# Optimization experiments

Hardware: AMD Instinct MI355X
Metric: run time of the kernel (lower is better)

## Reference

```python
import jax, jax.numpy as jnp
import numpy as np
import math

D_MODEL = 1024
N_HEADS = 16
DK = D_MODEL // N_HEADS


def setup_inputs() -> dict:
    key = jax.random.key(0)
    kx, kqkv, kproj = jax.random.split(key, 3)
    B, T = 4, 2048
    x = jax.random.normal(kx, (B, T, D_MODEL), dtype=jnp.float32)
    # torch Linear weight is [out, in]; y = x @ W.T
    W_qkv = jax.random.normal(kqkv, (3 * D_MODEL, D_MODEL), dtype=jnp.float32) * (1.0 / math.sqrt(D_MODEL))
    W_proj = jax.random.normal(kproj, (D_MODEL, D_MODEL), dtype=jnp.float32) * (1.0 / math.sqrt(D_MODEL))
    return {"x": x, "W_qkv": W_qkv, "W_proj": W_proj}


def reference(x, W_qkv, W_proj):
    B, T, D = x.shape
    qkv = jnp.einsum("btd,ed->bte", x, W_qkv)  # [B,T,3D]
    q, k, v = jnp.split(qkv, 3, axis=-1)
    # [B,T,D] -> [B,H,T,dk]
    def heads(t):
        return t.reshape(B, T, N_HEADS, DK).transpose(0, 2, 1, 3)
    q, k, v = heads(q), heads(k), heads(v)
    scale = 1.0 / math.sqrt(DK)
    att = jnp.einsum("bhqd,bhkd->bhqk", q, k) * scale  # [B,H,T,T]
    att = jax.nn.softmax(att, axis=-1)
    out = jnp.einsum("bhqk,bhkd->bhqd", att, v)  # [B,H,T,dk]
    out = out.transpose(0, 2, 1, 3).reshape(B, T, D)
    return jnp.einsum("btd,ed->bte", out, W_proj)
```

## Files before the change

### kernel.cpp

```cpp
#include <hip/hip_runtime.h>
#include <hip/hip_bf16.h>

#define D_MODEL 1024
#define N_HEADS 16
#define DK 64
#define B_SZ 4
#define T_SEQ 2048
#define M_ROWS (B_SZ * T_SEQ)
#define QK_SCALE_LOG2 0.18033688f

#define XN ((size_t)M_ROWS * D_MODEL)
#define WQ ((size_t)3 * D_MODEL * D_MODEL)
#define WP ((size_t)D_MODEL * D_MODEL)

typedef short bf16x8 __attribute__((ext_vector_type(8)));
typedef float f32x4  __attribute__((ext_vector_type(4)));

__device__ inline unsigned short f32_to_bf16(float f) {
    union { float f; unsigned int u; } v; v.f = f;
    unsigned int r = v.u + 0x7fff + ((v.u >> 16) & 1);
    return (unsigned short)(r >> 16);
}
__device__ inline unsigned int pack_bf16x2(float a, float b) {
    __hip_bfloat162 t = __float22bfloat162_rn(make_float2(a, b));
    union { __hip_bfloat162 v; unsigned int u; } c; c.v = t;
    return c.u;
}

__global__ __launch_bounds__(256) void cast_all(
    const float* __restrict__ x, const float* __restrict__ W_qkv,
    const float* __restrict__ W_proj,
    unsigned short* __restrict__ xb, unsigned short* __restrict__ wqb,
    unsigned short* __restrict__ wpb)
{
    const size_t total = (XN + WQ + WP) / 4;
    for (size_t i4 = blockIdx.x * 256 + threadIdx.x; i4 < total;
         i4 += gridDim.x * 256) {
        const size_t i = i4 * 4;
        const float* src; unsigned short* dst; float sc = 1.0f; size_t off;
        if (i < XN) {
            src = x; dst = xb; off = i;
        } else if (i < XN + WQ) {
            off = i - XN; src = W_qkv; dst = wqb;
            if (off < (size_t)D_MODEL * D_MODEL) sc = QK_SCALE_LOG2;
        } else {
            off = i - XN - WQ; src = W_proj; dst = wpb;
        }
        float4 v = *(const float4*)(src + off);
        ushort4 h;
        h.x = f32_to_bf16(v.x * sc); h.y = f32_to_bf16(v.y * sc);
        h.z = f32_to_bf16(v.z * sc); h.w = f32_to_bf16(v.w * sc);
        *(ushort4*)(dst + off) = h;
    }
}

template <typename OutT, bool FUSE_VT>
__global__ __launch_bounds__(256, 4) void gemm_bf16_nt(
    const unsigned short* __restrict__ A, const unsigned short* __restrict__ B,
    OutT* __restrict__ C, unsigned short* __restrict__ vt,
    int M, int N, int K)
{
    __shared__ __align__(16) unsigned short sA[128 * 64];
    __shared__ __align__(16) unsigned short sB[128 * 64];

    const int t    = threadIdx.x;
    const int wave = t >> 6;
    const int lane = t & 63;
    const int l15  = lane & 15;
    const int quad = lane >> 4;
    const int swz  = l15 & 7;

    const int cpx = gridDim.x >> 3;
    const int wg  = (blockIdx.x & 7) * cpx + (blockIdx.x >> 3);
    const int nbm = M >> 7;
    const int n0  = (wg / nbm) * 128;
    const int m0  = (wg % nbm) * 128;

    const unsigned short* gplane = (wave < 2) ? A : B;
    unsigned short* lplane = (wave < 2) ? sA : sB;
    const int row0 = ((wave < 2) ? m0 : n0) + (wave & 1) * 64;
    unsigned short* lbase = lplane + (wave & 1) * 4096;
    const int rsub = lane >> 3;
    const int cg   = (lane & 7) ^ rsub;
    const unsigned short* gbase =
        gplane + (size_t)(row0 + rsub) * K + cg * 8;

    f32x4 acc[4][4];
#pragma unroll
    for (int i = 0; i < 4; ++i)
#pragma unroll
        for (int j = 0; j < 4; ++j) acc[i][j] = (f32x4){0.f, 0.f, 0.f, 0.f};

    const int wr = (wave >> 1) * 64;
    const int wc = (wave & 1) * 64;

    for (int k0 = 0; k0 < K; k0 += 64) {
#pragma unroll
        for (int i = 0; i < 8; ++i) {
            __builtin_amdgcn_global_load_lds(
                (const __attribute__((address_space(1))) unsigned int*)
                    (gbase + k0 + (size_t)(i * 8) * K),
                (__attribute__((address_space(3))) unsigned int*)
                    (lbase + i * 512),
                16, 0, 0);
        }
        __syncthreads();

#pragma unroll
        for (int kk = 0; kk < 2; ++kk) {
            bf16x8 a[4], b[4];
            const int ch = kk * 4 + quad;
            const int co = (ch ^ swz) * 8;
#pragma unroll
            for (int f = 0; f < 4; ++f) {
                a[f] = *(const bf16x8*)&sA[(wr + f * 16 + l15) * 64 + co];
                b[f] = *(const bf16x8*)&sB[(wc + f * 16 + l15) * 64 + co];
            }
#pragma unroll
            for (int mi = 0; mi < 4; ++mi)
#pragma unroll
                for (int ni = 0; ni < 4; ++ni)
                    acc[mi][ni] = __builtin_amdgcn_mfma_f32_16x16x32_bf16(
                        a[mi], b[ni], acc[mi][ni], 0, 0, 0);
        }
        __syncthreads();
    }

    if constexpr (FUSE_VT) {
        if (n0 >= 2 * D_MODEL) {
            const int bb   = m0 >> 11;
            const int tile = (m0 & 2047) >> 7;
            const int hA   = (n0 + wc - 2 * D_MODEL) >> 6;
            unsigned short* vtile =
                vt + ((size_t)((bb * N_HEADS + hA) * (T_SEQ / 128) + tile))
                     * (16 * 64 * 8);
            const int chi = (wr >> 6) * 8;
#pragma unroll
            for (int cc = 0; cc < 2; ++cc) {
                const int c   = chi + cc * 4 + quad;
                const int mi0 = 2 * cc;
#pragma unroll
                for (int ni = 0; ni < 4; ++ni) {
                    const int d = ni * 16 + l15;
                    uint4 p;
                    p.x = pack_bf16x2(acc[mi0][ni][0],     acc[mi0][ni][1]);
                    p.y = pack_bf16x2(acc[mi0][ni][2],     acc[mi0][ni][3]);
                    p.z = pack_bf16x2(acc[mi0 + 1][ni][0], acc[mi0 + 1][ni][1]);
                    p.w = pack_bf16x2(acc[mi0 + 1][ni][2], acc[mi0 + 1][ni][3]);
                    *(uint4*)(vtile + (c * 64 + d) * 8) = p;
                }
            }
            return;
        }
    }

#pragma unroll
    for (int mi = 0; mi < 4; ++mi)
#pragma unroll
        for (int r = 0; r < 4; ++r) {
            OutT* crow =
                C + (size_t)(m0 + wr + mi * 16 + quad * 4 + r) * N + n0 + wc + l15;
#pragma unroll
            for (int ni = 0; ni < 4; ++ni) {
                if constexpr (sizeof(OutT) == 2)
                    crow[ni * 16] = (OutT)f32_to_bf16(acc[mi][ni][r]);
                else
                    crow[ni * 16] = (OutT)acc[mi][ni][r];
            }
        }
}

__global__ __launch_bounds__(256, 4) void attn_mfma(
    const unsigned short* __restrict__ qkvb,
    const unsigned short* __restrict__ vt,
    unsigned short* __restrict__ ob)
{
    __shared__ __align__(16) unsigned short Ksw[2][128 * 64];

    const int t    = threadIdx.x;
    const int wave = t >> 6;
    const int lane = t & 63;
    const int l15  = t & 15;
    const int quad = lane >> 4;
    const int swz  = l15 & 7;

    const int b  = blockIdx.z;
    const int h  = blockIdx.y;
    const int q0 = blockIdx.x * 128;

    bf16x8 qa[2][2];
#pragma unroll
    for (int qs = 0; qs < 2; ++qs) {
        const unsigned short* qrow =
            qkvb + ((size_t)(b * T_SEQ) + q0 + wave * 32 + qs * 16 + l15)
                   * (3 * D_MODEL) + h * DK;
        qa[qs][0] = *(const bf16x8*)(qrow + quad * 8);
        qa[qs][1] = *(const bf16x8*)(qrow + 32 + quad * 8);
    }

    f32x4 O[2][4], Lacc[2];
#pragma unroll
    for (int qs = 0; qs < 2; ++qs) {
        Lacc[qs] = (f32x4){0.f, 0.f, 0.f, 0.f};
#pragma unroll
        for (int nd = 0; nd < 4; ++nd) O[qs][nd] = (f32x4){0.f, 0.f, 0.f, 0.f};
    }

    const short one_bf = (short)0x3F80;
    const bf16x8 ones8 = {one_bf, one_bf, one_bf, one_bf,
                          one_bf, one_bf, one_bf, one_bf};

    const unsigned short* kbase =
        qkvb + (size_t)(b * T_SEQ) * (3 * D_MODEL) + D_MODEL + h * DK;
    const unsigned short* vbase =
        vt + (size_t)(b * N_HEADS + h) * DK * T_SEQ;

    const int krl  = wave * 32 + (lane >> 3);
    const int kcol = ((lane & 7) ^ (lane >> 3)) * 8;

#pragma unroll
    for (int i = 0; i < 4; ++i) {
        const int rk = krl + i * 8;
        __builtin_amdgcn_global_load_lds(
            (const __attribute__((address_space(1))) unsigned int*)
                (kbase + (size_t)rk * (3 * D_MODEL) + kcol),
            (__attribute__((address_space(3))) unsigned int*)
                (&Ksw[0][(wave * 4 + i) * 512]),
            16, 0, 0);
    }

    const int NT = T_SEQ / 128;
    for (int tile = 0; tile < NT; ++tile) {
        __syncthreads();

        if (tile + 1 < NT) {
            const int c0n = (tile + 1) * 128;
            const int nb  = (tile + 1) & 1;
#pragma unroll
            for (int i = 0; i < 4; ++i) {
                const int rk = krl + i * 8;
                __builtin_amdgcn_global_load_lds(
                    (const __attribute__((address_space(1))) unsigned int*)
                        (kbase + (size_t)(c0n + rk) * (3 * D_MODEL) + kcol),
                    (__attribute__((address_space(3))) unsigned int*)
                        (&Ksw[nb][(wave * 4 + i) * 512]),
                    16, 0, 0);
            }
        }

        const int cb = tile & 1;
        const unsigned short* vtile = vbase + (size_t)tile * (16 * 64 * 8);
        const unsigned short* vlane = vtile + quad * 512 + l15 * 8;
#pragma unroll
        for (int half = 0; half < 2; ++half) {
            f32x4 S[2][4];
#pragma unroll
            for (int qs = 0; qs < 2; ++qs)
#pragma unroll
                for (int nf = 0; nf < 4; ++nf) S[qs][nf] = (f32x4){0.f, 0.f, 0.f, 0.f};

            __builtin_amdgcn_s_setprio(1);
#pragma unroll
            for (int ks = 0; ks < 2; ++ks) {
                const int ch = ks * 4 + quad;
#pragma unroll
                for (int nf = 0; nf < 4; ++nf) {
                    const int row = half * 64 + nf * 16 + l15;
                    const bf16x8 kf =
                        *(const bf16x8*)&Ksw[cb][row * 64 + ((ch ^ swz) * 8)];
                    S[0][nf] = __builtin_amdgcn_mfma_f32_16x16x32_bf16(
                        kf, qa[0][ks], S[0][nf], 0, 0, 0);
                    S[1][nf] = __builtin_amdgcn_mfma_f32_16x16x32_bf16(
                        kf, qa[1][ks], S[1][nf], 0, 0, 0);
                }
            }
            __builtin_amdgcn_s_setprio(0);

#pragma unroll
            for (int gl = 0; gl < 2; ++gl) {
                bf16x8 pf[2];
#pragma unroll
                for (int qs = 0; qs < 2; ++qs) {
                    union { uint4 u; bf16x8 v; } cv;
                    const f32x4 s0 = S[qs][2 * gl];
                    const f32x4 s1 = S[qs][2 * gl + 1];
                    cv.u.x = pack_bf16x2(__builtin_amdgcn_exp2f(s0[0]),
                                         __builtin_amdgcn_exp2f(s0[1]));
                    cv.u.y = pack_bf16x2(__builtin_amdgcn_exp2f(s0[2]),
                                         __builtin_amdgcn_exp2f(s0[3]));
                    cv.u.z = pack_bf16x2(__builtin_amdgcn_exp2f(s1[0]),
                                         __builtin_amdgcn_exp2f(s1[1]));
                    cv.u.w = pack_bf16x2(__builtin_amdgcn_exp2f(s1[2]),
                                         __builtin_amdgcn_exp2f(s1[3]));
                    pf[qs] = cv.v;
                }
                const int g = half * 2 + gl;
                const unsigned short* vptr = vlane + (size_t)g * 2048;
                __builtin_amdgcn_s_setprio(1);
#pragma unroll
                for (int nd = 0; nd < 4; ++nd) {
                    const bf16x8 vb = *(const bf16x8*)(vptr + nd * 128);
                    O[0][nd] = __builtin_amdgcn_mfma_f32_16x16x32_bf16(
                        pf[0], vb, O[0][nd], 0, 0, 0);
                    O[1][nd] = __builtin_amdgcn_mfma_f32_16x16x32_bf16(
                        pf[1], vb, O[1][nd], 0, 0, 0);
                }
                Lacc[0] = __builtin_amdgcn_mfma_f32_16x16x32_bf16(
                    pf[0], ones8, Lacc[0], 0, 0, 0);
                Lacc[1] = __builtin_amdgcn_mfma_f32_16x16x32_bf16(
                    pf[1], ones8, Lacc[1], 0, 0, 0);
                __builtin_amdgcn_s_setprio(0);
            }
        }
    }

#pragma unroll
    for (int qs = 0; qs < 2; ++qs)
#pragma unroll
        for (int r = 0; r < 4; ++r) {
            const float invl = 1.0f / Lacc[qs][r];
            const size_t rowbase =
                ((size_t)(b * T_SEQ) + q0 + wave * 32 + qs * 16 + quad * 4 + r)
                * D_MODEL + h * DK + l15;
#pragma unroll
            for (int nd = 0; nd < 4; ++nd)
                ob[rowbase + nd * 16] = f32_to_bf16(O[qs][nd][r] * invl);
        }
}

extern "C" void kernel_launch(void* const* d_in, const int* in_sizes, int n_in,
                              void* d_out, int out_size, void* d_ws, size_t ws_size,
                              hipStream_t stream)
{
    const float* x      = (const float*)d_in[0];
    const float* W_qkv  = (const float*)d_in[1];
    const float* W_proj = (const float*)d_in[2];
    float* out = (float*)d_out;

    unsigned short* xb   = (unsigned short*)d_ws;
    unsigned short* wqb  = xb + XN;
    unsigned short* wpb  = wqb + WQ;
    unsigned short* qkvb = wpb + WP;
    unsigned short* vtb  = qkvb + (size_t)M_ROWS * 3 * D_MODEL;
    unsigned short* ab   = xb;

    dim3 blk(256);
    cast_all<<<1024, blk, 0, stream>>>(x, W_qkv, W_proj, xb, wqb, wpb);

    gemm_bf16_nt<unsigned short, true>
        <<<dim3((3 * D_MODEL / 128) * (M_ROWS / 128)), blk, 0, stream>>>(
        xb, wqb, qkvb, vtb, M_ROWS, 3 * D_MODEL, D_MODEL);

    attn_mfma<<<dim3(T_SEQ / 128, N_HEADS, B_SZ), blk, 0, stream>>>(
        qkvb, vtb, ab);

    gemm_bf16_nt<float, false>
        <<<dim3((D_MODEL / 128) * (M_ROWS / 128)), blk, 0, stream>>>(
        ab, wpb, out, nullptr, M_ROWS, D_MODEL, D_MODEL);
}
```

Before: 271.4 us.

## Double-buffer LDS tiles in bf16 GEMM and prefetch next K-slice

The projection GEMM now uses two LDS buffers per operand. It issues the global-to-LDS loads for the next 64-wide K slice right after the barrier, so they overlap with the MFMAs on the current slice, and it drops one of the two barriers per iteration. It also swaps the workgroup-to-tile mapping so consecutive workgroups walk along N within an M row, and raises wave priority around the MFMA block with s_setprio. LDS use per block doubles to 64 KB, which may cut the number of resident blocks per CU below the launch-bounds target.

```diff
diff --git a/kernel.cpp b/kernel.cpp
--- a/kernel.cpp
+++ b/kernel.cpp
@@ -60,8 +60,8 @@
     OutT* __restrict__ C, unsigned short* __restrict__ vt,
     int M, int N, int K)
 {
-    __shared__ __align__(16) unsigned short sA[128 * 64];
-    __shared__ __align__(16) unsigned short sB[128 * 64];
+    __shared__ __align__(16) unsigned short sA[2][128 * 64];
+    __shared__ __align__(16) unsigned short sB[2][128 * 64];
 
     const int t    = threadIdx.x;
     const int wave = t >> 6;
@@ -72,14 +72,14 @@
 
     const int cpx = gridDim.x >> 3;
     const int wg  = (blockIdx.x & 7) * cpx + (blockIdx.x >> 3);
-    const int nbm = M >> 7;
-    const int n0  = (wg / nbm) * 128;
-    const int m0  = (wg % nbm) * 128;
+    const int nbx = N >> 7;
+    const int n0  = (wg % nbx) * 128;
+    const int m0  = (wg / nbx) * 128;
 
     const unsigned short* gplane = (wave < 2) ? A : B;
-    unsigned short* lplane = (wave < 2) ? sA : sB;
+    unsigned short* lplane = (wave < 2) ? sA[0] : sB[0];
     const int row0 = ((wave < 2) ? m0 : n0) + (wave & 1) * 64;
-    unsigned short* lbase = lplane + (wave & 1) * 4096;
+    const int loff = (wave & 1) * 4096;
     const int rsub = lane >> 3;
     const int cg   = (lane & 7) ^ rsub;
     const unsigned short* gbase =
@@ -94,18 +94,35 @@
     const int wr = (wave >> 1) * 64;
     const int wc = (wave & 1) * 64;
 
-    for (int k0 = 0; k0 < K; k0 += 64) {
-#pragma unroll
-        for (int i = 0; i < 8; ++i) {
-            __builtin_amdgcn_global_load_lds(
-                (const __attribute__((address_space(1))) unsigned int*)
-                    (gbase + k0 + (size_t)(i * 8) * K),
-                (__attribute__((address_space(3))) unsigned int*)
-                    (lbase + i * 512),
-                16, 0, 0);
-        }
+    const int nk = K >> 6;
+#pragma unroll
+    for (int i = 0; i < 8; ++i) {
+        __builtin_amdgcn_global_load_lds(
+            (const __attribute__((address_space(1))) unsigned int*)
+                (gbase + (size_t)(i * 8) * K),
+            (__attribute__((address_space(3))) unsigned int*)
+                (lplane + loff + i * 512),
+            16, 0, 0);
+    }
+
+    for (int kt = 0; kt < nk; ++kt) {
         __syncthreads();
 
+        if (kt + 1 < nk) {
+            const int k0n = (kt + 1) << 6;
+            const int nb  = (kt + 1) & 1;
+#pragma unroll
+            for (int i = 0; i < 8; ++i) {
+                __builtin_amdgcn_global_load_lds(
+                    (const __attribute__((address_space(1))) unsigned int*)
+                        (gbase + k0n + (size_t)(i * 8) * K),
+                    (__attribute__((address_space(3))) unsigned int*)
+                        (lplane + nb * 8192 + loff + i * 512),
+                    16, 0, 0);
+            }
+        }
+
+        const int cb = kt & 1;
 #pragma unroll
         for (int kk = 0; kk < 2; ++kk) {
             bf16x8 a[4], b[4];
@@ -113,17 +130,18 @@
             const int co = (ch ^ swz) * 8;
 #pragma unroll
             for (int f = 0; f < 4; ++f) {
-                a[f] = *(const bf16x8*)&sA[(wr + f * 16 + l15) * 64 + co];
-                b[f] = *(const bf16x8*)&sB[(wc + f * 16 + l15) * 64 + co];
-            }
+                a[f] = *(const bf16x8*)&sA[cb][(wr + f * 16 + l15) * 64 + co];
+                b[f] = *(const bf16x8*)&sB[cb][(wc + f * 16 + l15) * 64 + co];
+            }
+            __builtin_amdgcn_s_setprio(1);
 #pragma unroll
             for (int mi = 0; mi < 4; ++mi)
 #pragma unroll
                 for (int ni = 0; ni < 4; ++ni)
                     acc[mi][ni] = __builtin_amdgcn_mfma_f32_16x16x32_bf16(
                         a[mi], b[ni], acc[mi][ni], 0, 0, 0);
-        }
-        __syncthreads();
+            __builtin_amdgcn_s_setprio(0);
+        }
     }
 
     if constexpr (FUSE_VT) {
```

Result: faster. 247.2 us (-8.9%).
